# Kernel tuning notes

Hardware: AMD Instinct MI355X
Metric: run time of the kernel (lower is better)

The kernel has to match this reference:

```python
import jax, jax.numpy as jnp
import numpy as np

N_LEVELS = 256  # 2**8

def setup_inputs() -> dict:
    key = jax.random.key(0)
    k1, k2, k3, k4 = jax.random.split(key, 4)
    x = jax.random.normal(k1, (4, 4096, 4096), dtype=jnp.float32)
    # medians increase across MAD iterations (inliers are zeroed each round)
    medians = jnp.sort(jax.random.uniform(k2, (10,), dtype=jnp.float32, minval=0.5, maxval=4.0))
    deltas = jax.random.uniform(k3, (10,), dtype=jnp.float32, minval=0.005, maxval=0.05)
    zero_points = jnp.round(jax.random.uniform(k4, (10,), dtype=jnp.float32) * (N_LEVELS - 1))
    return {"x": x, "medians": medians, "deltas": deltas, "zero_points": zero_points}

def reference(x, medians, deltas, zero_points):
    G = medians.shape[0]  # number of MAD groups (== max_iters kept)
    x_abs = jnp.abs(x)
    # group id = number of medians <= |x|, clamped — same as the torch loop of comparisons
    grp = jnp.zeros(x.shape, dtype=jnp.int32)
    for i in range(G):  # G is small and static (10)
        grp = grp + (x_abs >= medians[i]).astype(jnp.int32)
    grp = jnp.clip(grp, 0, G - 1)
    d = deltas[grp]
    zp = zero_points[grp]
    x_quant = jnp.clip(jnp.round(x / d) + zp, 0.0, N_LEVELS - 1)
    return (x_quant - zp) * d
```

## Files before the change

kernel.cpp:

```cpp
#include <hip/hip_runtime.h>

#define G 10
#define NLEV_MINUS_1 255.0f

__global__ __launch_bounds__(256) void madq_kernel(
    const float* __restrict__ x,
    const float* __restrict__ medians,
    const float* __restrict__ deltas,
    const float* __restrict__ zps,
    float* __restrict__ out,
    int n4)
{
    int idx = blockIdx.x * blockDim.x + threadIdx.x;
    if (idx >= n4) return;

    float m[G], dd[G], zz[G];
#pragma unroll
    for (int i = 0; i < G; ++i) {
        m[i]  = medians[i];
        dd[i] = deltas[i];
        zz[i] = zps[i];
    }

    const float4* x4 = (const float4*)x;
    float4*       o4 = (float4*)out;
    float4 v = x4[idx];

    float in[4] = {v.x, v.y, v.z, v.w};
    float ou[4];
#pragma unroll
    for (int e = 0; e < 4; ++e) {
        float xv = in[e];
        float xa = fabsf(xv);
        float d  = dd[0];
        float zp = zz[0];
#pragma unroll
        for (int i = 1; i < G; ++i) {
            bool c = xa >= m[i - 1];
            d  = c ? dd[i] : d;
            zp = c ? zz[i] : zp;
        }
        float q = rintf(xv / d) + zp;
        q = fminf(fmaxf(q, 0.0f), NLEV_MINUS_1);
        ou[e] = (q - zp) * d;
    }
    o4[idx] = make_float4(ou[0], ou[1], ou[2], ou[3]);
}

extern "C" void kernel_launch(void* const* d_in, const int* in_sizes, int n_in,
                              void* d_out, int out_size, void* d_ws, size_t ws_size,
                              hipStream_t stream) {
    const float* x       = (const float*)d_in[0];
    const float* medians = (const float*)d_in[1];
    const float* deltas  = (const float*)d_in[2];
    const float* zps     = (const float*)d_in[3];
    float*       out     = (float*)d_out;

    int n  = in_sizes[0];
    int n4 = n / 4;
    const int block = 256;
    int grid = (n4 + block - 1) / block;
    madq_kernel<<<grid, block, 0, stream>>>(x, medians, deltas, zps, out, n4);
}
```

Before: 418.7 us.

## Process four float4 per thread with nontemporal loads/stores and scalar params

Each thread now handles four float4 vectors with a strided coalesced layout, issuing all loads up front to raise memory-level parallelism. Loads and stores use nontemporal hints to avoid cache pollution for streaming data. The small parameter tables are read through readfirstlane so they live in scalar registers. This quarters the grid size and raises register pressure per thread.

Result: slower. 429.3 us (+2.5%).

```diff
diff --git a/kernel.cpp b/kernel.cpp
--- a/kernel.cpp
+++ b/kernel.cpp
@@ -1,50 +1,59 @@
 #include <hip/hip_runtime.h>
 
 #define G 10
-#define NLEV_MINUS_1 255.0f
+
+typedef float vf4 __attribute__((ext_vector_type(4)));
+
+__device__ __forceinline__ float sload(const float* p, int i) {
+    return __uint_as_float(__builtin_amdgcn_readfirstlane(__float_as_uint(p[i])));
+}
 
 __global__ __launch_bounds__(256) void madq_kernel(
-    const float* __restrict__ x,
+    const vf4* __restrict__ x4,
     const float* __restrict__ medians,
     const float* __restrict__ deltas,
     const float* __restrict__ zps,
-    float* __restrict__ out,
+    vf4* __restrict__ o4,
     int n4)
 {
-    int idx = blockIdx.x * blockDim.x + threadIdx.x;
-    if (idx >= n4) return;
+    const int base = blockIdx.x * (256 * 4) + threadIdx.x;
 
-    float m[G], dd[G], zz[G];
+    vf4 v[4];
+    bool ok[4];
 #pragma unroll
-    for (int i = 0; i < G; ++i) {
-        m[i]  = medians[i];
-        dd[i] = deltas[i];
-        zz[i] = zps[i];
+    for (int j = 0; j < 4; ++j) {
+        int idx = base + j * 256;
+        ok[j] = idx < n4;
+        if (ok[j]) v[j] = __builtin_nontemporal_load(&x4[idx]);
     }
 
-    const float4* x4 = (const float4*)x;
-    float4*       o4 = (float4*)out;
-    float4 v = x4[idx];
+    float m[G - 1], dd[G], zz[G];
+#pragma unroll
+    for (int i = 0; i < G - 1; ++i) m[i] = sload(medians, i);
+#pragma unroll
+    for (int i = 0; i < G; ++i) { dd[i] = sload(deltas, i); zz[i] = sload(zps, i); }
 
-    float in[4] = {v.x, v.y, v.z, v.w};
-    float ou[4];
 #pragma unroll
-    for (int e = 0; e < 4; ++e) {
-        float xv = in[e];
-        float xa = fabsf(xv);
-        float d  = dd[0];
-        float zp = zz[0];
+    for (int j = 0; j < 4; ++j) {
+        if (!ok[j]) continue;
+        vf4 r;
 #pragma unroll
-        for (int i = 1; i < G; ++i) {
-            bool c = xa >= m[i - 1];
-            d  = c ? dd[i] : d;
-            zp = c ? zz[i] : zp;
+        for (int e = 0; e < 4; ++e) {
+            float xv = v[j][e];
+            float xa = fabsf(xv);
+            float d = dd[0], zp = zz[0];
+#pragma unroll
+            for (int i = 1; i < G; ++i) {
+                bool c = xa >= m[i - 1];
+                d  = c ? dd[i] : d;
+                zp = c ? zz[i] : zp;
+            }
+            float q = rintf(xv / d) + zp;
+            q = fminf(fmaxf(q, 0.0f), 255.0f);
+            r[e] = (q - zp) * d;
         }
-        float q = rintf(xv / d) + zp;
-        q = fminf(fmaxf(q, 0.0f), NLEV_MINUS_1);
-        ou[e] = (q - zp) * d;
+        __builtin_nontemporal_store(r, &o4[base + j * 256]);
     }
-    o4[idx] = make_float4(ou[0], ou[1], ou[2], ou[3]);
 }
 
 extern "C" void kernel_launch(void* const* d_in, const int* in_sizes, int n_in,
@@ -59,6 +68,8 @@
     int n  = in_sizes[0];
     int n4 = n / 4;
     const int block = 256;
-    int grid = (n4 + block - 1) / block;
-    madq_kernel<<<grid, block, 0, stream>>>(x, medians, deltas, zps, out, n4);
+    const int per_block = block * 4;
+    int grid = (n4 + per_block - 1) / per_block;
+    madq_kernel<<<grid, block, 0, stream>>>(
+        (const vf4*)x, medians, deltas, zps, (vf4*)out, n4);
 }
```
